# Kernel optimization log

Hardware: AMD Instinct MI355X
Metric: run time of the kernel (lower is better)

Reference implementation:

```python
import jax, jax.numpy as jnp
import numpy as np

N_ATOMS = 100000; E_ATOMS = 200000; N_AMINO = 10240; E_AMINO = 20480; B = 512
D_IN = 40; D_E = 11; H1 = 20; H2 = 20; H3 = 20; D_AA = 8; H_ARMA = 128; K = 3; T = 7
F1 = 256; F2 = 128; F3 = 64


def setup_inputs() -> dict:
    key = jax.random.key(0)
    ks = jax.random.split(key, 40)
    s = 0.05
    inp = {}
    inp['x'] = jax.random.normal(ks[0], (N_ATOMS, D_IN), dtype=jnp.float32)
    inp['edge_index'] = jax.random.randint(ks[1], (2, E_ATOMS), 0, N_ATOMS, dtype=jnp.int32)
    inp['edge_attr'] = jax.random.normal(ks[2], (E_ATOMS, D_E), dtype=jnp.float32)
    inp['monomer_labels'] = jax.random.randint(ks[3], (N_ATOMS,), 0, N_AMINO, dtype=jnp.int32)
    inp['aminoacids_features'] = jax.random.normal(ks[4], (N_AMINO, D_AA), dtype=jnp.float32)
    inp['amino_edge_index'] = jax.random.randint(ks[5], (2, E_AMINO), 0, N_AMINO, dtype=jnp.int32)
    inp['amino_batch'] = jnp.sort(jax.random.randint(ks[6], (N_AMINO,), 0, B, dtype=jnp.int32))
    # NNConv params: edge-MLP (Linear(D_E, in*out)), root weight, bias
    inp['nn1_w'] = jax.random.normal(ks[7], (D_E, D_IN * H1)) * s
    inp['nn1_b'] = jax.random.normal(ks[8], (D_IN * H1,)) * s
    inp['root1'] = jax.random.normal(ks[9], (D_IN, H1)) * s
    inp['b1'] = jax.random.normal(ks[10], (H1,)) * s
    inp['nn2_w'] = jax.random.normal(ks[11], (D_E, H1 * H2)) * s
    inp['nn2_b'] = jax.random.normal(ks[12], (H1 * H2,)) * s
    inp['root2'] = jax.random.normal(ks[13], (H1, H2)) * s
    inp['b2'] = jax.random.normal(ks[14], (H2,)) * s
    inp['nn3_w'] = jax.random.normal(ks[15], (D_E, H2 * H3)) * s
    inp['nn3_b'] = jax.random.normal(ks[16], (H2 * H3,)) * s
    inp['root3'] = jax.random.normal(ks[17], (H2, H3)) * s
    inp['b3'] = jax.random.normal(ks[18], (H3,)) * s
    # ARMAConv params (K stacks, T layers, shared_weights=False)
    F_ARMA_IN = H3 + D_AA
    inp['arma_init'] = jax.random.normal(ks[19], (K, F_ARMA_IN, H_ARMA)) * s
    inp['arma_w'] = jax.random.normal(ks[20], (T - 1, K, H_ARMA, H_ARMA)) * s
    inp['arma_root'] = jax.random.normal(ks[21], (T, K, F_ARMA_IN, H_ARMA)) * s
    inp['arma_bias'] = jax.random.normal(ks[22], (T, K, 1, H_ARMA)) * s
    # FCN head
    inp['l1_w'] = jax.random.normal(ks[23], (H_ARMA, F1)) * s
    inp['l1_b'] = jax.random.normal(ks[24], (F1,)) * s
    inp['l2_w'] = jax.random.normal(ks[25], (F1, F2)) * s
    inp['l2_b'] = jax.random.normal(ks[26], (F2,)) * s
    inp['l3_w'] = jax.random.normal(ks[27], (F2, F3)) * s
    inp['l3_b'] = jax.random.normal(ks[28], (F3,)) * s
    inp['l4_w'] = jax.random.normal(ks[29], (F3, 1)) * s
    inp['l4_b'] = jax.random.normal(ks[30], (1,)) * s
    return inp


def _nnconv(x, ei, ea, w_nn, b_nn, root, bias, out_dim):
    # PyG NNConv (aggr='add'): out_i = x_i @ root + sum_{j->i} x_j @ W(e_ji) + bias
    E, d_in = ea.shape[0], x.shape[1]
    W = (ea @ w_nn + b_nn).reshape(E, d_in, out_dim)  # per-edge weight matrices
    msg = jnp.einsum('ei,eio->eo', x[ei[0]], W)       # gather + batched matvec
    agg = jax.ops.segment_sum(msg, ei[1], num_segments=x.shape[0])
    return x @ root + agg + bias


def _arma(x, ei, init_w, w, root_w, bias):
    # PyG ARMAConv: sym-normalized adjacency (no self loops), K stacks, T layers, ReLU act
    N = x.shape[0]
    deg = jax.ops.segment_sum(jnp.ones(ei.shape[1], x.dtype), ei[1], num_segments=N)
    dinv = jnp.where(deg > 0, deg ** -0.5, 0.0)
    norm = dinv[ei[0]] * dinv[ei[1]]  # [E_amino]
    out = None
    for t in range(T):
        h = jnp.einsum('nf,kfo->kno', x, init_w) if t == 0 else jnp.einsum('knf,kfo->kno', out, w[t - 1])
        msg = h[:, ei[0], :] * norm[None, :, None]
        h = jax.vmap(lambda m: jax.ops.segment_sum(m, ei[1], num_segments=N))(msg)
        h = h + jnp.einsum('nf,kfo->kno', x, root_w[t]) + bias[t]
        out = jax.nn.relu(h)
    return out.mean(0)  # mean over stacks


def reference(x, edge_index, edge_attr, monomer_labels, aminoacids_features,
              amino_edge_index, amino_batch,
              nn1_w, nn1_b, root1, b1, nn2_w, nn2_b, root2, b2, nn3_w, nn3_b, root3, b3,
              arma_init, arma_w, arma_root, arma_bias,
              l1_w, l1_b, l2_w, l2_b, l3_w, l3_b, l4_w, l4_b):
    h = jax.nn.relu(_nnconv(x, edge_index, edge_attr, nn1_w, nn1_b, root1, b1, H1))
    h = jax.nn.relu(_nnconv(h, edge_index, edge_attr, nn2_w, nn2_b, root2, b2, H2))
    h = jax.nn.relu(_nnconv(h, edge_index, edge_attr, nn3_w, nn3_b, root3, b3, H3))
    # per-graph loop flattened: atoms -> amino-acid sum readout (graphs disjoint)
    aa = jax.ops.segment_sum(h, monomer_labels, num_segments=N_AMINO)
    aa = jnp.concatenate([aa, aminoacids_features], axis=1)  # [N_AMINO, H3+8]
    aa = jax.nn.relu(_arma(aa, amino_edge_index, arma_init, arma_w, arma_root, arma_bias))
    g = jax.ops.segment_sum(aa, amino_batch, num_segments=B)  # per-graph sum readout
    p = jax.nn.relu(g @ l1_w + l1_b)  # dropout is identity in eval mode
    p = jax.nn.relu(p @ l2_w + l2_b)
    p = jax.nn.relu(p @ l3_w + l3_b)
    return (p @ l4_w + l4_b).reshape(-1)
```

## Files before the change

### kernel.cpp

```cpp
#include <hip/hip_runtime.h>

#define N_ATOMS 100000
#define E_ATOMS 200000
#define N_AMINO 10240
#define E_AMINO 20480
#define NGRAPH 512
#define DIN0 40
#define D_E 11
#define HD 20
#define D_AA 8
#define HA 128
#define KS 3
#define TL 7
#define F1 256
#define F2 128
#define F3 64
#define NTILE 16
#define ECAP 64
#define EAW 12

typedef unsigned short u16;
typedef unsigned int u32;
typedef __attribute__((ext_vector_type(8))) short short8;
typedef __attribute__((ext_vector_type(4))) float f32x4;

__device__ __forceinline__ float b2f(u16 u) {
    union { u32 i; float f; } v; v.i = ((u32)u) << 16; return v.f;
}
__device__ __forceinline__ u16 f2b(float f) {
    union { float f; u32 i; } v; v.f = f;
    u32 x = v.i;
    return (u16)((x + (((x >> 16) & 1u) + 0x7fffu)) >> 16);
}

#define MB1_ELEMS 15360
#define MB2_ELEMS 7680
#define PREP0_N (MB1_ELEMS + 2 * MB2_ELEMS + N_AMINO * D_AA + 2 * N_ATOMS + 2 * N_AMINO)
__global__ __launch_bounds__(256) void k_prep0(
    const float* __restrict__ w1, const float* __restrict__ b1,
    const float* __restrict__ w2, const float* __restrict__ b2,
    const float* __restrict__ w3, const float* __restrict__ b3,
    u16* __restrict__ Mb1, u16* __restrict__ Mb2, u16* __restrict__ Mb3,
    const float* __restrict__ af, float* __restrict__ aa,
    int* __restrict__ cs, int* __restrict__ cd,
    int* __restrict__ ca, int* __restrict__ cl) {
    int t = blockIdx.x * 256 + threadIdx.x;
    if (t < MB1_ELEMS) {
        int kb = t / 7680, rem = t % 7680;
        int c = rem >> 5, qj = rem & 31;
        int krow = kb * 32 + qj;
        float v = 0.f;
        if (krow < DIN0)
            v = (c < 220) ? w1[(c / 20) * 800 + krow * 20 + (c % 20)]
                          : b1[krow * 20 + (c - 220)];
        Mb1[t] = f2b(v);
    } else if (t < MB1_ELEMS + MB2_ELEMS) {
        int tt = t - MB1_ELEMS;
        int c = tt >> 5, qj = tt & 31;
        float v = 0.f;
        if (qj < HD)
            v = (c < 220) ? w2[(c / 20) * 400 + qj * 20 + (c % 20)]
                          : b2[qj * 20 + (c - 220)];
        Mb2[tt] = f2b(v);
    } else if (t < MB1_ELEMS + 2 * MB2_ELEMS) {
        int tt = t - MB1_ELEMS - MB2_ELEMS;
        int c = tt >> 5, qj = tt & 31;
        float v = 0.f;
        if (qj < HD)
            v = (c < 220) ? w3[(c / 20) * 400 + qj * 20 + (c % 20)]
                          : b3[qj * 20 + (c - 220)];
        Mb3[tt] = f2b(v);
    } else if (t < MB1_ELEMS + 2 * MB2_ELEMS + N_AMINO * D_AA) {
        int idx = t - MB1_ELEMS - 2 * MB2_ELEMS, m = idx / D_AA, j = idx % D_AA;
        aa[m * 28 + HD + j] = af[idx];
    } else {
        int z = t - MB1_ELEMS - 2 * MB2_ELEMS - N_AMINO * D_AA;
        if (z < N_ATOMS) cs[z] = 0;
        else if (z < 2 * N_ATOMS) cd[z - N_ATOMS] = 0;
        else if (z < 2 * N_ATOMS + N_AMINO) ca[z - 2 * N_ATOMS] = 0;
        else if (z < 2 * N_ATOMS + 2 * N_AMINO) cl[z - 2 * N_ATOMS - N_AMINO] = 0;
    }
}

#define WP0_ELEMS (KS * 8192)
#define WP1_ELEMS (6 * KS * 20480)
__global__ __launch_bounds__(256) void k_cvtwp2(
    const float* __restrict__ ai, const float* __restrict__ aw,
    const float* __restrict__ arw, u16* __restrict__ Wp) {
    int g = blockIdx.x * 256 + threadIdx.x;
    if (g < WP0_ELEMS) {
        int k = g / 8192, r = g % 8192;
        int kb = r >> 12, rem = r & 4095;
        int c = rem >> 5, qj = rem & 31;
        int krow = kb * 32 + qj;
        float v = 0.f;
        if (krow < 28)      v = ai[((size_t)k * 28 + krow) * HA + c];
        else if (krow < 56) v = arw[((size_t)k * 28 + (krow - 28)) * HA + c];
        Wp[g] = f2b(v);
    } else if (g < WP0_ELEMS + WP1_ELEMS) {
        int gg = g - WP0_ELEMS;
        int mat = gg / 20480, r = gg % 20480;
        int kb = r / 4096, rem = r & 4095;
        int c = rem >> 5, qj = rem & 31;
        int krow = kb * 32 + qj;
        int tm1 = mat / KS, k = mat % KS;
        float v = 0.f;
        if (krow < 128)      v = aw[((size_t)mat * 128 + krow) * HA + c];
        else if (krow < 156) v = arw[(((size_t)(tm1 + 1) * KS + k) * 28 + (krow - 128)) * HA + c];
        Wp[g] = f2b(v);
    }
}

#define NBS 98
#define NBA 10

__global__ __launch_bounds__(256) void k_csr_count(
    const int* __restrict__ esrc, const int* __restrict__ edst,
    const int* __restrict__ adst, const int* __restrict__ lbl,
    int* __restrict__ cs, int* __restrict__ cd,
    int* __restrict__ ca, int* __restrict__ cl) {
    int t = blockIdx.x * 256 + threadIdx.x;
    if (t < E_ATOMS) atomicAdd(cs + esrc[t], 1);
    else if (t < 2 * E_ATOMS) atomicAdd(cd + edst[t - E_ATOMS], 1);
    else if (t < 2 * E_ATOMS + E_AMINO) atomicAdd(ca + adst[t - 2 * E_ATOMS], 1);
    else if (t < 2 * E_ATOMS + E_AMINO + N_ATOMS) atomicAdd(cl + lbl[t - 2 * E_ATOMS - E_AMINO], 1);
}
__device__ __forceinline__ void seg_decode(int bx, int* blk, int* n, int* which) {
    if (bx < NBS)            { *which = 0; *blk = bx;             *n = N_ATOMS; }
    else if (bx < 2 * NBS)   { *which = 1; *blk = bx - NBS;       *n = N_ATOMS; }
    else if (bx < 2 * NBS + NBA) { *which = 2; *blk = bx - 2 * NBS; *n = N_AMINO; }
    else                     { *which = 3; *blk = bx - 2 * NBS - NBA; *n = N_AMINO; }
}
__global__ __launch_bounds__(256) void k_scan1(
    const int* __restrict__ cs, int* __restrict__ soff,
    const int* __restrict__ cd, int* __restrict__ doff,
    const int* __restrict__ ca, int* __restrict__ aoff,
    const int* __restrict__ cl, int* __restrict__ loff,
    int* __restrict__ bsum) {
    int blk, n, which;
    seg_decode(blockIdx.x, &blk, &n, &which);
    const int* c = which == 0 ? cs : which == 1 ? cd : which == 2 ? ca : cl;
    int* o = which == 0 ? soff : which == 1 ? doff : which == 2 ? aoff : loff;
    int tx = threadIdx.x, lane = tx & 63, w = tx >> 6;
    int i0 = blk * 1024 + tx * 4;
    int v[4];
#pragma unroll
    for (int q = 0; q < 4; ++q) v[q] = (i0 + q < n) ? c[i0 + q] : 0;
    int s = v[0] + v[1] + v[2] + v[3];
    int inc = s;
#pragma unroll
    for (int d = 1; d < 64; d <<= 1) {
        int u = __shfl_up(inc, d, 64);
        if (lane >= d) inc += u;
    }
    __shared__ int wsum[4];
    if (lane == 63) wsum[w] = inc;
    __syncthreads();
    int wo = 0;
    for (int i = 0; i < w; ++i) wo += wsum[i];
    int run = wo + inc - s;
#pragma unroll
    for (int q = 0; q < 4; ++q) {
        if (i0 + q < n) o[i0 + q] = run;
        run += v[q];
    }
    if (tx == 255) bsum[blockIdx.x] = wo + inc;
}
__global__ __launch_bounds__(128) void k_scan2(
    int* __restrict__ bsum, int* __restrict__ soff, int* __restrict__ doff,
    int* __restrict__ aoff, int* __restrict__ loff) {
    int bx = blockIdx.x;
    int nb   = (bx < 2) ? NBS : NBA;
    int base = (bx == 0) ? 0 : (bx == 1) ? NBS : (bx == 2) ? 2 * NBS : 2 * NBS + NBA;
    int* b = bsum + base;
    int tx = threadIdx.x, lane = tx & 63;
    int v = (tx < nb) ? b[tx] : 0;
    int inc = v;
#pragma unroll
    for (int d = 1; d < 64; d <<= 1) {
        int u = __shfl_up(inc, d, 64);
        if (lane >= d) inc += u;
    }
    __shared__ int w0;
    if (tx == 63) w0 = inc;
    __syncthreads();
    int excl = inc - v + ((tx >= 64) ? w0 : 0);
    if (tx < nb) b[tx] = excl;
    if (tx == nb - 1) {
        int tot = excl + v;
        if (bx == 0) soff[N_ATOMS] = tot;
        else if (bx == 1) doff[N_ATOMS] = tot;
        else if (bx == 2) aoff[N_AMINO] = tot;
        else loff[N_AMINO] = tot;
    }
}
__global__ __launch_bounds__(256) void k_scan3(
    int* __restrict__ soff, int* __restrict__ doff,
    int* __restrict__ aoff, int* __restrict__ loff,
    const int* __restrict__ bsum,
    int* __restrict__ us, int* __restrict__ ud,
    int* __restrict__ ua, int* __restrict__ ul) {
    int blk, n, which;
    seg_decode(blockIdx.x, &blk, &n, &which);
    int* o = which == 0 ? soff : which == 1 ? doff : which == 2 ? aoff : loff;
    int* cu = which == 0 ? us : which == 1 ? ud : which == 2 ? ua : ul;
    int add = bsum[blockIdx.x];
    int i0 = blk * 1024 + threadIdx.x * 4;
#pragma unroll
    for (int q = 0; q < 4; ++q)
        if (i0 + q < n) { int val = o[i0 + q] + add; o[i0 + q] = val; cu[i0 + q] = val; }
}
__global__ __launch_bounds__(256) void k_csr_fill(
    const int* __restrict__ esrc, const int* __restrict__ edst,
    const float* __restrict__ ea,
    int* __restrict__ us, int* __restrict__ srcP, u16* __restrict__ eaP,
    int* __restrict__ ud, int* __restrict__ dslot,
    const int* __restrict__ aei, int* __restrict__ ua, int* __restrict__ aeid,
    const int* __restrict__ aoff, float* __restrict__ nrm,
    const int* __restrict__ lbl, int* __restrict__ ul, int* __restrict__ lnid) {
    int t = blockIdx.x * 256 + threadIdx.x;
    if (t < E_ATOMS) {
        int jj = atomicAdd(us + esrc[t], 1);
        srcP[jj] = esrc[t];
        const float* e0 = ea + (size_t)t * D_E;
        u16* e1 = eaP + (size_t)jj * EAW;
#pragma unroll
        for (int k = 0; k < D_E; ++k) e1[k] = f2b(e0[k]);
        e1[D_E] = f2b(1.0f);
        int p = atomicAdd(ud + edst[t], 1);
        dslot[p] = jj;
    } else if (t < E_ATOMS + E_AMINO) {
        int e = t - E_ATOMS;
        int p = atomicAdd(ua + aei[E_AMINO + e], 1);
        aeid[p] = e;
    } else if (t < E_ATOMS + 2 * E_AMINO) {
        int e = t - E_ATOMS - E_AMINO;
        int s = aei[e], d = aei[E_AMINO + e];
        int ds = aoff[s + 1] - aoff[s], dd = aoff[d + 1] - aoff[d];
        float a = ds > 0 ? rsqrtf((float)ds) : 0.f;
        float b = dd > 0 ? rsqrtf((float)dd) : 0.f;
        nrm[e] = a * b;
    } else if (t < E_ATOMS + 2 * E_AMINO + N_ATOMS) {
        int n = t - E_ATOMS - 2 * E_AMINO;
        int p = atomicAdd(ul + lbl[n], 1);
        lnid[p] = n;
    }
}

template <int DIN, int KB, bool RAW>
__global__ __launch_bounds__(256, 6) void nnconv_edge10(
    const void* __restrict__ xin, const u16* __restrict__ eaP,
    const int* __restrict__ srcP, const int* __restrict__ soff,
    const u16* __restrict__ Mb, u16* __restrict__ msg) {
    constexpr int KPAD = KB * 32;
    __shared__ __align__(16) float y3[NTILE * 240];
    __shared__ __align__(16) u16 As[NTILE * KPAD];
    __shared__ __align__(16) float eaS[ECAP * 12];
    __shared__ int srcS[ECAP];
    int tx = threadIdx.x;
    int n0 = blockIdx.x * NTILE;
    int j0 = soff[n0], j1 = soff[n0 + NTILE];
    for (int i = tx; i < NTILE * KPAD; i += 256) {
        int node = i / KPAD, k = i % KPAD;
        u16 v = 0;
        if (k < DIN)
            v = RAW ? f2b(((const float*)xin)[(size_t)(n0 + node) * DIN + k])
                    : ((const u16*)xin)[(size_t)(n0 + node) * DIN + k];
        As[i] = v;
    }
    {
        int cn0 = j1 - j0; if (cn0 > ECAP) cn0 = ECAP;
        for (int i = tx; i < cn0; i += 256) srcS[i] = srcP[j0 + i] - n0;
        const u32* eg = (const u32*)(eaP + (size_t)j0 * EAW);
        for (int i = tx; i < cn0 * 6; i += 256) {
            u32 pv = eg[i];
            eaS[2 * i]     = b2f((u16)(pv & 0xffff));
            eaS[2 * i + 1] = b2f((u16)(pv >> 16));
        }
    }
    __syncthreads();
    {
        int wave = tx >> 6, lane = tx & 63;
        int m = lane & 15, q = lane >> 4;
        short8 aF[KB];
#pragma unroll
        for (int kb = 0; kb < KB; ++kb)
            aF[kb] = *(const short8*)&As[m * KPAD + kb * 32 + q * 8];
        for (int ct = wave; ct < 15; ct += 4) {
            int c0 = ct * 16;
            f32x4 acc = {0.f, 0.f, 0.f, 0.f};
#pragma unroll
            for (int kb = 0; kb < KB; ++kb) {
                short8 bF = *(const short8*)(Mb + (size_t)kb * 7680 + (size_t)(c0 + m) * 32 + q * 8);
                acc = __builtin_amdgcn_mfma_f32_16x16x32_bf16(aF[kb], bF, acc, 0, 0, 0);
            }
            int c = c0 + m;
            int slot = (c < 220) ? (c % 20) * 12 + c / 20 : (c - 220) * 12 + 11;
#pragma unroll
            for (int r = 0; r < 4; ++r)
                y3[(q * 4 + r) * 240 + slot] = acc[r];
        }
    }
    __syncthreads();
    int c0 = j0;
    while (true) {
        int cn = j1 - c0; if (cn > ECAP) cn = ECAP;
        for (int p = tx; p < cn * 20; p += 256) {
            int e = p / 20, o = p - e * 20;
            const float4* ev = (const float4*)&eaS[e * 12];
            const float4* yr = (const float4*)&y3[srcS[e] * 240 + o * 12];
            float4 e0 = ev[0], e1 = ev[1], e2 = ev[2];
            float4 q0 = yr[0], q1 = yr[1], q2 = yr[2];
            float mv = e0.x * q0.x + e0.y * q0.y + e0.z * q0.z + e0.w * q0.w
                     + e1.x * q1.x + e1.y * q1.y + e1.z * q1.z + e1.w * q1.w
                     + e2.x * q2.x + e2.y * q2.y + e2.z * q2.z + e2.w * q2.w;
            msg[(size_t)(c0 + e) * 20 + o] = f2b(mv);
        }
        c0 += cn;
        if (c0 >= j1) break;
        __syncthreads();
        int cm = j1 - c0; if (cm > ECAP) cm = ECAP;
        for (int i = tx; i < cm; i += 256) srcS[i] = srcP[c0 + i] - n0;
        const u32* eg = (const u32*)(eaP + (size_t)c0 * EAW);
        for (int i = tx; i < cm * 6; i += 256) {
            u32 pv = eg[i];
            eaS[2 * i]     = b2f((u16)(pv & 0xffff));
            eaS[2 * i + 1] = b2f((u16)(pv >> 16));
        }
        __syncthreads();
    }
}

template <int DIN, bool RAW>
__global__ __launch_bounds__(256) void nnconv_reduce(
    const void* __restrict__ xin, const float* __restrict__ root,
    const float* __restrict__ bias, const int* __restrict__ doff,
    const int* __restrict__ dslot, const u16* __restrict__ msg,
    u16* __restrict__ hout) {
    __shared__ float Rl[DIN * HD + HD];
    for (int t = threadIdx.x; t < DIN * HD; t += 256) Rl[t] = root[t];
    if (threadIdx.x < HD) Rl[DIN * HD + threadIdx.x] = bias[threadIdx.x];
    __syncthreads();
    int t = blockIdx.x * 256 + threadIdx.x;
    if (t >= N_ATOMS * HD) return;
    int n = t / HD, o = t % HD;
    float acc = Rl[DIN * HD + o];
    int j1 = doff[n + 1];
    for (int j = doff[n]; j < j1; ++j)
        acc += b2f(msg[(size_t)dslot[j] * 20 + o]);
    const float* xf = (const float*)xin + (size_t)n * DIN;
    const u16*   xb = (const u16*)xin + (size_t)n * DIN;
#pragma unroll
    for (int i = 0; i < DIN; ++i)
        acc += (RAW ? xf[i] : b2f(xb[i])) * Rl[i * HD + o];
    hout[t] = f2b(fmaxf(acc, 0.f));
}

__global__ __launch_bounds__(256) void aa_gather(
    const u16* __restrict__ h3, const int* __restrict__ loff,
    const int* __restrict__ lnid, float* __restrict__ aa) {
    int t = blockIdx.x * 256 + threadIdx.x;
    if (t >= N_AMINO * HD) return;
    int m = t / HD, o = t % HD;
    float s = 0.f;
    int j1 = loff[m + 1];
    for (int j = loff[m]; j < j1; ++j)
        s += b2f(h3[(size_t)lnid[j] * HD + o]);
    aa[m * 28 + o] = s;
}

__global__ __launch_bounds__(256) void k_gaa(
    const float* __restrict__ aa, const int* __restrict__ aoff,
    const int* __restrict__ aeid, const int* __restrict__ aei,
    const float* __restrict__ nrm, u16* __restrict__ A0) {
    int t = blockIdx.x * 256 + threadIdx.x;
    if (t >= N_AMINO * 64) return;
    int n = t >> 6, c = t & 63;
    float v = 0.f;
    if (c < 28) {
        int j1 = aoff[n + 1];
        for (int jj = aoff[n]; jj < j1; ++jj) {
            int e = aeid[jj], s = aei[e];
            v += nrm[e] * aa[(size_t)s * 28 + c];
        }
    } else if (c < 56) {
        v = aa[(size_t)n * 28 + (c - 28)];
    }
    A0[t] = f2b(v);
}

__global__ __launch_bounds__(256) void arma_l0(
    const u16* __restrict__ A0, const u16* __restrict__ Wp0,
    const float* __restrict__ abi, u16* __restrict__ O, size_t kstride) {
    int wave = threadIdx.x >> 6, lane = threadIdx.x & 63;
    int k = blockIdx.y;
    const u16* W = Wp0 + (size_t)k * 8192;
    u16* Ok = O + (size_t)k * kstride;
    const float* bk = abi + (size_t)k * HA;
    int n0 = (blockIdx.x * 4 + wave) * 16;
    int m = lane & 15, q = lane >> 4;
    short8 aF[2];
#pragma unroll
    for (int kb = 0; kb < 2; ++kb)
        aF[kb] = *(const short8*)(A0 + (size_t)(n0 + m) * 64 + kb * 32 + q * 8);
#pragma unroll
    for (int ct = 0; ct < 8; ++ct) {
        int c0 = ct * 16;
        float b = bk[c0 + m];
        f32x4 acc = {b, b, b, b};
#pragma unroll
        for (int kb = 0; kb < 2; ++kb) {
            short8 bF = *(const short8*)(W + (size_t)((kb * 128 + c0 + m) * 32 + q * 8));
            acc = __builtin_amdgcn_mfma_f32_16x16x32_bf16(aF[kb], bF, acc, 0, 0, 0);
        }
#pragma unroll
        for (int r = 0; r < 4; ++r)
            Ok[(size_t)(n0 + q * 4 + r) * HA + c0 + m] = f2b(fmaxf(acc[r], 0.f));
    }
}

__global__ __launch_bounds__(256) void arma_lt(
    const u16* __restrict__ Oprev, const u16* __restrict__ Wm,
    const float* __restrict__ abit, const float* __restrict__ aa,
    const int* __restrict__ aoff, const int* __restrict__ aeid,
    const int* __restrict__ aei, const float* __restrict__ nrm,
    u16* __restrict__ Onext, size_t kstride) {
    __shared__ __align__(16) u16 As[64 * 160];
    int tx = threadIdx.x;
    int k = blockIdx.y;
    int n0b = blockIdx.x * 64;
    const u16* Op = Oprev + (size_t)k * kstride;
    const u16* W  = Wm + (size_t)k * 20480;
    for (int i = tx; i < 1024; i += 256) {
        int nl = i >> 4, cb = i & 15;
        int n = n0b + nl;
        int j1 = aoff[n + 1];
        float a0 = 0.f, a1 = 0.f, a2 = 0.f, a3 = 0.f;
        float a4 = 0.f, a5 = 0.f, a6 = 0.f, a7 = 0.f;
        for (int jj = aoff[n]; jj < j1; ++jj) {
            int e = aeid[jj], s = aei[e];
            float nm = nrm[e];
            uint4 hv = *(const uint4*)(Op + (size_t)s * HA + cb * 8);
            a0 += nm * b2f((u16)(hv.x & 0xffff));
            a1 += nm * b2f((u16)(hv.x >> 16));
            a2 += nm * b2f((u16)(hv.y & 0xffff));
            a3 += nm * b2f((u16)(hv.y >> 16));
            a4 += nm * b2f((u16)(hv.z & 0xffff));
            a5 += nm * b2f((u16)(hv.z >> 16));
            a6 += nm * b2f((u16)(hv.w & 0xffff));
            a7 += nm * b2f((u16)(hv.w >> 16));
        }
        uint4 pk;
        pk.x = (u32)f2b(a0) | ((u32)f2b(a1) << 16);
        pk.y = (u32)f2b(a2) | ((u32)f2b(a3) << 16);
        pk.z = (u32)f2b(a4) | ((u32)f2b(a5) << 16);
        pk.w = (u32)f2b(a6) | ((u32)f2b(a7) << 16);
        *(uint4*)&As[nl * 160 + cb * 8] = pk;
    }
    {
        int nl = tx >> 2, cb = tx & 3;
        int n = n0b + nl;
        float av[8];
#pragma unroll
        for (int j = 0; j < 8; ++j) {
            int c = cb * 8 + j;
            av[j] = (c < 28) ? aa[(size_t)n * 28 + c] : 0.f;
        }
        uint4 pk;
        pk.x = (u32)f2b(av[0]) | ((u32)f2b(av[1]) << 16);
        pk.y = (u32)f2b(av[2]) | ((u32)f2b(av[3]) << 16);
        pk.z = (u32)f2b(av[4]) | ((u32)f2b(av[5]) << 16);
        pk.w = (u32)f2b(av[6]) | ((u32)f2b(av[7]) << 16);
        *(uint4*)&As[nl * 160 + 128 + cb * 8] = pk;
    }
    __syncthreads();
    int wave = tx >> 6, lane = tx & 63;
    int m = lane & 15, q = lane >> 4;
    int wl = wave * 16 + m;
    short8 aF[5];
#pragma unroll
    for (int kb = 0; kb < 5; ++kb)
        aF[kb] = *(const short8*)&As[wl * 160 + kb * 32 + q * 8];
    int n0 = n0b + wave * 16;
    u16* On = Onext + (size_t)k * kstride;
    const float* bk = abit + (size_t)k * HA;
#pragma unroll
    for (int ct = 0; ct < 8; ++ct) {
        int c0 = ct * 16;
        float b = bk[c0 + m];
        f32x4 acc = {b, b, b, b};
#pragma unroll
        for (int kb = 0; kb < 5; ++kb) {
            short8 bF = *(const short8*)(W + (size_t)((kb * 128 + c0 + m) * 32 + q * 8));
            acc = __builtin_amdgcn_mfma_f32_16x16x32_bf16(aF[kb], bF, acc, 0, 0, 0);
        }
#pragma unroll
        for (int r = 0; r < 4; ++r)
            On[(size_t)(n0 + q * 4 + r) * HA + c0 + m] = f2b(fmaxf(acc[r], 0.f));
    }
}

__global__ __launch_bounds__(256) void head2(
    const u16* __restrict__ O, size_t kstride, const int* __restrict__ bat,
    const float* __restrict__ l1w, const float* __restrict__ l1b,
    const float* __restrict__ l2w, const float* __restrict__ l2b,
    const float* __restrict__ l3w, const float* __restrict__ l3b,
    const float* __restrict__ l4w, const float* __restrict__ l4b,
    float* __restrict__ outp) {
    __shared__ float sg[HA], sp1[F1], sp2[F2], sp3[F3];
    int b = blockIdx.x, tx = threadIdx.x;
    int lo = 0, hi = N_AMINO;
    while (lo < hi) { int mid = (lo + hi) >> 1; if (bat[mid] < b) lo = mid + 1; else hi = mid; }
    int s = lo;
    lo = 0; hi = N_AMINO;
    while (lo < hi) { int mid = (lo + hi) >> 1; if (bat[mid] < b + 1) lo = mid + 1; else hi = mid; }
    int e = lo;
    if (tx < HA) {
        float acc = 0.f;
        for (int n = s; n < e; ++n)
            acc += b2f(O[(size_t)n * HA + tx]) + b2f(O[kstride + (size_t)n * HA + tx])
                 + b2f(O[2 * kstride + (size_t)n * HA + tx]);
        sg[tx] = acc * (1.f / 3.f);
    }
    __syncthreads();
    {   float acc = l1b[tx];
        for (int f = 0; f < HA; ++f) acc += sg[f] * l1w[f * F1 + tx];
        sp1[tx] = fmaxf(acc, 0.f); }
    __syncthreads();
    if (tx < F2) {
        float acc = l2b[tx];
        for (int f = 0; f < F1; ++f) acc += sp1[f] * l2w[f * F2 + tx];
        sp2[tx] = fmaxf(acc, 0.f); }
    __syncthreads();
    if (tx < F3) {
        float acc = l3b[tx];
        for (int f = 0; f < F2; ++f) acc += sp2[f] * l3w[f * F3 + tx];
        sp3[tx] = fmaxf(acc, 0.f); }
    __syncthreads();
    if (tx < 64) {
        float p = sp3[tx] * l4w[tx];
        for (int off = 32; off > 0; off >>= 1) p += __shfl_down(p, off, 64);
        if (tx == 0) outp[b] = p + l4b[0];
    }
}

#define OFF_M1    ((size_t)0)
#define OFF_M2    ((size_t)38400)
#define OFF_M3    ((size_t)57600)
#define OFF_AOFF  ((size_t)76800)
#define OFF_AEID  ((size_t)118016)
#define OFF_NRM   ((size_t)199936)
#define OFF_AA    ((size_t)281856)
#define OFF_HA    ((size_t)2891008)
#define OFF_HB    ((size_t)6891008)
#define OFF_MSG   ((size_t)10891008)
#define OFF_SOFF  ((size_t)18891008)
#define OFF_DOFF  ((size_t)19291136)
#define OFF_DSLOT ((size_t)19691264)
#define OFF_LOFF  ((size_t)20491264)
#define OFF_LNID  ((size_t)20532480)
#define OFF_CS    ((size_t)20932480)
#define OFF_CD    ((size_t)21332480)
#define OFF_CA    ((size_t)21732480)
#define OFF_CL    ((size_t)21773440)
#define OFF_US    ((size_t)21814400)
#define OFF_UD    ((size_t)22214400)
#define OFF_UA    ((size_t)22614400)
#define OFF_UL    ((size_t)22655360)
#define OFF_BSUM  ((size_t)22696320)
#define OFF_EAP   ((size_t)22697216)
#define OFF_SRCP  ((size_t)27497216)
#define OFF_WP    ((size_t)28297216)
#define OFF_OB    ((size_t)2891008)
#define OFF_A0    ((size_t)10891008)
#define OFF_OA    ((size_t)18619648)

extern "C" void kernel_launch(void* const* d_in, const int* in_sizes, int n_in,
                              void* d_out, int out_size, void* d_ws, size_t ws_size,
                              hipStream_t stream) {
    (void)in_sizes; (void)n_in; (void)out_size; (void)ws_size;
    const float* x   = (const float*)d_in[0];
    const int*   ei  = (const int*)d_in[1];
    const float* ea  = (const float*)d_in[2];
    const int*   lbl = (const int*)d_in[3];
    const float* af  = (const float*)d_in[4];
    const int*   aei = (const int*)d_in[5];
    const int*   bat = (const int*)d_in[6];
    const float* nn1w = (const float*)d_in[7];  const float* nn1b = (const float*)d_in[8];
    const float* rt1  = (const float*)d_in[9];  const float* b1   = (const float*)d_in[10];
    const float* nn2w = (const float*)d_in[11]; const float* nn2b = (const float*)d_in[12];
    const float* rt2  = (const float*)d_in[13]; const float* b2   = (const float*)d_in[14];
    const float* nn3w = (const float*)d_in[15]; const float* nn3b = (const float*)d_in[16];
    const float* rt3  = (const float*)d_in[17]; const float* b3   = (const float*)d_in[18];
    const float* ai   = (const float*)d_in[19]; const float* aw   = (const float*)d_in[20];
    const float* arw  = (const float*)d_in[21]; const float* abi  = (const float*)d_in[22];
    const float* l1w  = (const float*)d_in[23]; const float* l1b  = (const float*)d_in[24];
    const float* l2w  = (const float*)d_in[25]; const float* l2b  = (const float*)d_in[26];
    const float* l3w  = (const float*)d_in[27]; const float* l3b  = (const float*)d_in[28];
    const float* l4w  = (const float*)d_in[29]; const float* l4b  = (const float*)d_in[30];
    float* outp = (float*)d_out;

    char* ws = (char*)d_ws;
    u16*   Mb1   = (u16*)(ws + OFF_M1);
    u16*   Mb2   = (u16*)(ws + OFF_M2);
    u16*   Mb3   = (u16*)(ws + OFF_M3);
    int*   aoff  = (int*)(ws + OFF_AOFF);
    int*   aeid  = (int*)(ws + OFF_AEID);
    float* nrm   = (float*)(ws + OFF_NRM);
    float* aa    = (float*)(ws + OFF_AA);
    u16*   hA    = (u16*)(ws + OFF_HA);
    u16*   hB    = (u16*)(ws + OFF_HB);
    u16*   msg   = (u16*)(ws + OFF_MSG);
    int*   soff  = (int*)(ws + OFF_SOFF);
    int*   doff  = (int*)(ws + OFF_DOFF);
    int*   dslot = (int*)(ws + OFF_DSLOT);
    int*   loff  = (int*)(ws + OFF_LOFF);
    int*   lnid  = (int*)(ws + OFF_LNID);
    int*   cs    = (int*)(ws + OFF_CS);
    int*   cd    = (int*)(ws + OFF_CD);
    int*   ca    = (int*)(ws + OFF_CA);
    int*   cl    = (int*)(ws + OFF_CL);
    int*   us    = (int*)(ws + OFF_US);
    int*   ud    = (int*)(ws + OFF_UD);
    int*   ua    = (int*)(ws + OFF_UA);
    int*   ul    = (int*)(ws + OFF_UL);
    int*   bsum  = (int*)(ws + OFF_BSUM);
    u16*   eaP   = (u16*)(ws + OFF_EAP);
    int*   srcP  = (int*)(ws + OFF_SRCP);
    u16*   Wp    = (u16*)(ws + OFF_WP);
    u16*   A0    = (u16*)(ws + OFF_A0);
    u16*   OA    = (u16*)(ws + OFF_OA);
    u16*   OB    = (u16*)(ws + OFF_OB);

    const int* esrc = ei;
    const int* edst = ei + E_ATOMS;
    const int* adst = aei + E_AMINO;

    k_prep0<<<(PREP0_N + 255) / 256, 256, 0, stream>>>(
        nn1w, nn1b, nn2w, nn2b, nn3w, nn3b, Mb1, Mb2, Mb3, af, aa, cs, cd, ca, cl);
    k_cvtwp2<<<(WP0_ELEMS + WP1_ELEMS + 255) / 256, 256, 0, stream>>>(ai, aw, arw, Wp);
    k_csr_count<<<(2 * E_ATOMS + E_AMINO + N_ATOMS + 255) / 256, 256, 0, stream>>>(
        esrc, edst, adst, lbl, cs, cd, ca, cl);
    k_scan1<<<2 * NBS + 2 * NBA, 256, 0, stream>>>(cs, soff, cd, doff, ca, aoff, cl, loff, bsum);
    k_scan2<<<4, 128, 0, stream>>>(bsum, soff, doff, aoff, loff);
    k_scan3<<<2 * NBS + 2 * NBA, 256, 0, stream>>>(soff, doff, aoff, loff, bsum, us, ud, ua, ul);
    k_csr_fill<<<(E_ATOMS + 2 * E_AMINO + N_ATOMS + 255) / 256, 256, 0, stream>>>(
        esrc, edst, ea, us, srcP, eaP, ud, dslot, aei, ua, aeid, aoff, nrm, lbl, ul, lnid);

    const int GT = N_ATOMS / NTILE;
    const int GF = (N_ATOMS * HD + 255) / 256;
    nnconv_edge10<DIN0, 2, true ><<<GT, 256, 0, stream>>>(x,  eaP, srcP, soff, Mb1, msg);
    nnconv_reduce<DIN0, true ><<<GF, 256, 0, stream>>>(x,  rt1, b1, doff, dslot, msg, hA);
    nnconv_edge10<HD,   1, false><<<GT, 256, 0, stream>>>(hA, eaP, srcP, soff, Mb2, msg);
    nnconv_reduce<HD,   false><<<GF, 256, 0, stream>>>(hA, rt2, b2, doff, dslot, msg, hB);
    nnconv_edge10<HD,   1, false><<<GT, 256, 0, stream>>>(hB, eaP, srcP, soff, Mb3, msg);
    nnconv_reduce<HD,   false><<<GF, 256, 0, stream>>>(hB, rt3, b3, doff, dslot, msg, hA);
    aa_gather<<<(N_AMINO * HD + 255) / 256, 256, 0, stream>>>(hA, loff, lnid, aa);

    const size_t KH = (size_t)N_AMINO * HA;
    k_gaa<<<(N_AMINO * 64 + 255) / 256, 256, 0, stream>>>(aa, aoff, aeid, aei, nrm, A0);
    arma_l0<<<dim3(160, KS), 256, 0, stream>>>(A0, Wp, abi, OA, KH);
    for (int t = 1; t < TL; ++t) {
        const u16* Oin  = (t & 1) ? OA : OB;
        u16*       Oout = (t & 1) ? OB : OA;
        arma_lt<<<dim3(160, KS), 256, 0, stream>>>(
            Oin, Wp + WP0_ELEMS + (size_t)((t - 1) * KS) * 20480,
            abi + (size_t)t * KS * HA, aa, aoff, aeid, aei, nrm, Oout, KH);
    }
    head2<<<NGRAPH, 256, 0, stream>>>(OA, KH, bat, l1w, l1b, l2w, l2b,
                                      l3w, l3b, l4w, l4b, outp);
}
```

Before: 506.4 us.

## Fold root-weight transform into edge MFMA and write messages in destination order

Adds the root weight as an extra 20-column block in the per-layer MFMA weight matrix, so the edge kernel computes the self term plus bias per node and writes it to a new buffer. The reduce kernel no longer reloads node features or does the root dot product. Edge messages are now scattered straight to their destination-sorted slot (the CSR fill records each edge's slot), so the reduce reads messages contiguously instead of through an indirection array. The costs are two extra MFMA column tiles per edge block, scattered writes in the edge kernel, and the self term being rounded to bf16 before accumulation.

After: 469.3 us. 1.08x faster.

```diff
diff --git a/kernel.cpp b/kernel.cpp
--- a/kernel.cpp
+++ b/kernel.cpp
@@ -33,42 +33,48 @@
     return (u16)((x + (((x >> 16) & 1u) + 0x7fffu)) >> 16);
 }
 
-#define MB1_ELEMS 15360
-#define MB2_ELEMS 7680
+#define MB1_ELEMS 17408
+#define MB2_ELEMS 8704
 #define PREP0_N (MB1_ELEMS + 2 * MB2_ELEMS + N_AMINO * D_AA + 2 * N_ATOMS + 2 * N_AMINO)
 __global__ __launch_bounds__(256) void k_prep0(
-    const float* __restrict__ w1, const float* __restrict__ b1,
-    const float* __restrict__ w2, const float* __restrict__ b2,
-    const float* __restrict__ w3, const float* __restrict__ b3,
+    const float* __restrict__ w1, const float* __restrict__ nb1, const float* __restrict__ r1,
+    const float* __restrict__ w2, const float* __restrict__ nb2, const float* __restrict__ r2,
+    const float* __restrict__ w3, const float* __restrict__ nb3, const float* __restrict__ r3,
     u16* __restrict__ Mb1, u16* __restrict__ Mb2, u16* __restrict__ Mb3,
     const float* __restrict__ af, float* __restrict__ aa,
     int* __restrict__ cs, int* __restrict__ cd,
     int* __restrict__ ca, int* __restrict__ cl) {
     int t = blockIdx.x * 256 + threadIdx.x;
     if (t < MB1_ELEMS) {
-        int kb = t / 7680, rem = t % 7680;
+        int kb = t / 8704, rem = t % 8704;
         int c = rem >> 5, qj = rem & 31;
         int krow = kb * 32 + qj;
         float v = 0.f;
-        if (krow < DIN0)
-            v = (c < 220) ? w1[(c / 20) * 800 + krow * 20 + (c % 20)]
-                          : b1[krow * 20 + (c - 220)];
+        if (krow < DIN0) {
+            if (c < 220)      v = w1[(c / 20) * 800 + krow * 20 + (c % 20)];
+            else if (c < 240) v = nb1[krow * 20 + (c - 220)];
+            else if (c < 260) v = r1[krow * 20 + (c - 240)];
+        }
         Mb1[t] = f2b(v);
     } else if (t < MB1_ELEMS + MB2_ELEMS) {
         int tt = t - MB1_ELEMS;
         int c = tt >> 5, qj = tt & 31;
         float v = 0.f;
-        if (qj < HD)
-            v = (c < 220) ? w2[(c / 20) * 400 + qj * 20 + (c % 20)]
-                          : b2[qj * 20 + (c - 220)];
+        if (qj < HD) {
+            if (c < 220)      v = w2[(c / 20) * 400 + qj * 20 + (c % 20)];
+            else if (c < 240) v = nb2[qj * 20 + (c - 220)];
+            else if (c < 260) v = r2[qj * 20 + (c - 240)];
+        }
         Mb2[tt] = f2b(v);
     } else if (t < MB1_ELEMS + 2 * MB2_ELEMS) {
         int tt = t - MB1_ELEMS - MB2_ELEMS;
         int c = tt >> 5, qj = tt & 31;
         float v = 0.f;
-        if (qj < HD)
-            v = (c < 220) ? w3[(c / 20) * 400 + qj * 20 + (c % 20)]
-                          : b3[qj * 20 + (c - 220)];
+        if (qj < HD) {
+            if (c < 220)      v = w3[(c / 20) * 400 + qj * 20 + (c % 20)];
+            else if (c < 240) v = nb3[qj * 20 + (c - 220)];
+            else if (c < 260) v = r3[qj * 20 + (c - 240)];
+        }
         Mb3[tt] = f2b(v);
     } else if (t < MB1_ELEMS + 2 * MB2_ELEMS + N_AMINO * D_AA) {
         int idx = t - MB1_ELEMS - 2 * MB2_ELEMS, m = idx / D_AA, j = idx % D_AA;
@@ -214,7 +220,7 @@
     const int* __restrict__ esrc, const int* __restrict__ edst,
     const float* __restrict__ ea,
     int* __restrict__ us, int* __restrict__ srcP, u16* __restrict__ eaP,
-    int* __restrict__ ud, int* __restrict__ dslot,
+    int* __restrict__ ud, int* __restrict__ sdp,
     const int* __restrict__ aei, int* __restrict__ ua, int* __restrict__ aeid,
     const int* __restrict__ aoff, float* __restrict__ nrm,
     const int* __restrict__ lbl, int* __restrict__ ul, int* __restrict__ lnid) {
@@ -227,8 +233,7 @@
 #pragma unroll
         for (int k = 0; k < D_E; ++k) e1[k] = f2b(e0[k]);
         e1[D_E] = f2b(1.0f);
-        int p = atomicAdd(ud + edst[t], 1);
-        dslot[p] = jj;
+        sdp[jj] = atomicAdd(ud + edst[t], 1);
     } else if (t < E_ATOMS + E_AMINO) {
         int e = t - E_ATOMS;
         int p = atomicAdd(ua + aei[E_AMINO + e], 1);
@@ -248,15 +253,18 @@
 }
 
 template <int DIN, int KB, bool RAW>
-__global__ __launch_bounds__(256, 6) void nnconv_edge10(
+__global__ __launch_bounds__(256, 6) void nnconv_edge11(
     const void* __restrict__ xin, const u16* __restrict__ eaP,
-    const int* __restrict__ srcP, const int* __restrict__ soff,
-    const u16* __restrict__ Mb, u16* __restrict__ msg) {
+    const int* __restrict__ srcP, const int* __restrict__ sdp,
+    const int* __restrict__ soff, const u16* __restrict__ Mb,
+    const float* __restrict__ bnn, u16* __restrict__ msg,
+    u16* __restrict__ selfm) {
     constexpr int KPAD = KB * 32;
     __shared__ __align__(16) float y3[NTILE * 240];
     __shared__ __align__(16) u16 As[NTILE * KPAD];
     __shared__ __align__(16) float eaS[ECAP * 12];
     __shared__ int srcS[ECAP];
+    __shared__ int sdpS[ECAP];
     int tx = threadIdx.x;
     int n0 = blockIdx.x * NTILE;
     int j0 = soff[n0], j1 = soff[n0 + NTILE];
@@ -270,7 +278,10 @@
     }
     {
         int cn0 = j1 - j0; if (cn0 > ECAP) cn0 = ECAP;
-        for (int i = tx; i < cn0; i += 256) srcS[i] = srcP[j0 + i] - n0;
+        for (int i = tx; i < cn0; i += 256) {
+            srcS[i] = srcP[j0 + i] - n0;
+            sdpS[i] = sdp[j0 + i];
+        }
         const u32* eg = (const u32*)(eaP + (size_t)j0 * EAW);
         for (int i = tx; i < cn0 * 6; i += 256) {
             u32 pv = eg[i];
@@ -286,19 +297,26 @@
 #pragma unroll
         for (int kb = 0; kb < KB; ++kb)
             aF[kb] = *(const short8*)&As[m * KPAD + kb * 32 + q * 8];
-        for (int ct = wave; ct < 15; ct += 4) {
+        for (int ct = wave; ct < 17; ct += 4) {
             int c0 = ct * 16;
             f32x4 acc = {0.f, 0.f, 0.f, 0.f};
 #pragma unroll
             for (int kb = 0; kb < KB; ++kb) {
-                short8 bF = *(const short8*)(Mb + (size_t)kb * 7680 + (size_t)(c0 + m) * 32 + q * 8);
+                short8 bF = *(const short8*)(Mb + (size_t)kb * 8704 + (size_t)(c0 + m) * 32 + q * 8);
                 acc = __builtin_amdgcn_mfma_f32_16x16x32_bf16(aF[kb], bF, acc, 0, 0, 0);
             }
             int c = c0 + m;
-            int slot = (c < 220) ? (c % 20) * 12 + c / 20 : (c - 220) * 12 + 11;
-#pragma unroll
-            for (int r = 0; r < 4; ++r)
-                y3[(q * 4 + r) * 240 + slot] = acc[r];
+            if (c < 240) {
+                int slot = (c < 220) ? (c % 20) * 12 + c / 20 : (c - 220) * 12 + 11;
+#pragma unroll
+                for (int r = 0; r < 4; ++r)
+                    y3[(q * 4 + r) * 240 + slot] = acc[r];
+            } else if (c < 260) {
+                float bv = bnn[c - 240];
+#pragma unroll
+                for (int r = 0; r < 4; ++r)
+                    selfm[(size_t)(n0 + q * 4 + r) * 20 + (c - 240)] = f2b(acc[r] + bv);
+            }
         }
     }
     __syncthreads();
@@ -314,13 +332,16 @@
             float mv = e0.x * q0.x + e0.y * q0.y + e0.z * q0.z + e0.w * q0.w
                      + e1.x * q1.x + e1.y * q1.y + e1.z * q1.z + e1.w * q1.w
                      + e2.x * q2.x + e2.y * q2.y + e2.z * q2.z + e2.w * q2.w;
-            msg[(size_t)(c0 + e) * 20 + o] = f2b(mv);
+            msg[(size_t)sdpS[e] * 20 + o] = f2b(mv);
         }
         c0 += cn;
         if (c0 >= j1) break;
         __syncthreads();
         int cm = j1 - c0; if (cm > ECAP) cm = ECAP;
-        for (int i = tx; i < cm; i += 256) srcS[i] = srcP[c0 + i] - n0;
+        for (int i = tx; i < cm; i += 256) {
+            srcS[i] = srcP[c0 + i] - n0;
+            sdpS[i] = sdp[c0 + i];
+        }
         const u32* eg = (const u32*)(eaP + (size_t)c0 * EAW);
         for (int i = tx; i < cm * 6; i += 256) {
             u32 pv = eg[i];
@@ -331,28 +352,16 @@
     }
 }
 
-template <int DIN, bool RAW>
-__global__ __launch_bounds__(256) void nnconv_reduce(
-    const void* __restrict__ xin, const float* __restrict__ root,
-    const float* __restrict__ bias, const int* __restrict__ doff,
-    const int* __restrict__ dslot, const u16* __restrict__ msg,
-    u16* __restrict__ hout) {
-    __shared__ float Rl[DIN * HD + HD];
-    for (int t = threadIdx.x; t < DIN * HD; t += 256) Rl[t] = root[t];
-    if (threadIdx.x < HD) Rl[DIN * HD + threadIdx.x] = bias[threadIdx.x];
-    __syncthreads();
+__global__ __launch_bounds__(256) void nnconv_reduce2(
+    const u16* __restrict__ selfm, const int* __restrict__ doff,
+    const u16* __restrict__ msg, u16* __restrict__ hout) {
     int t = blockIdx.x * 256 + threadIdx.x;
     if (t >= N_ATOMS * HD) return;
-    int n = t / HD, o = t % HD;
-    float acc = Rl[DIN * HD + o];
+    int n = t / HD, o = t - n * HD;
+    float acc = b2f(selfm[t]);
     int j1 = doff[n + 1];
     for (int j = doff[n]; j < j1; ++j)
-        acc += b2f(msg[(size_t)dslot[j] * 20 + o]);
-    const float* xf = (const float*)xin + (size_t)n * DIN;
-    const u16*   xb = (const u16*)xin + (size_t)n * DIN;
-#pragma unroll
-    for (int i = 0; i < DIN; ++i)
-        acc += (RAW ? xf[i] : b2f(xb[i])) * Rl[i * HD + o];
+        acc += b2f(msg[(size_t)j * HD + o]);
     hout[t] = f2b(fmaxf(acc, 0.f));
 }
 
@@ -571,6 +580,7 @@
 #define OFF_EAP   ((size_t)22697216)
 #define OFF_SRCP  ((size_t)27497216)
 #define OFF_WP    ((size_t)28297216)
+#define OFF_SELFM ((size_t)29083648)
 #define OFF_OB    ((size_t)2891008)
 #define OFF_A0    ((size_t)10891008)
 #define OFF_OA    ((size_t)18619648)
@@ -613,7 +623,7 @@
     u16*   msg   = (u16*)(ws + OFF_MSG);
     int*   soff  = (int*)(ws + OFF_SOFF);
     int*   doff  = (int*)(ws + OFF_DOFF);
-    int*   dslot = (int*)(ws + OFF_DSLOT);
+    int*   sdp   = (int*)(ws + OFF_DSLOT);
     int*   loff  = (int*)(ws + OFF_LOFF);
     int*   lnid  = (int*)(ws + OFF_LNID);
     int*   cs    = (int*)(ws + OFF_CS);
@@ -628,6 +638,7 @@
     u16*   eaP   = (u16*)(ws + OFF_EAP);
     int*   srcP  = (int*)(ws + OFF_SRCP);
     u16*   Wp    = (u16*)(ws + OFF_WP);
+    u16*   selfm = (u16*)(ws + OFF_SELFM);
     u16*   A0    = (u16*)(ws + OFF_A0);
     u16*   OA    = (u16*)(ws + OFF_OA);
     u16*   OB    = (u16*)(ws + OFF_OB);
@@ -637,7 +648,8 @@
     const int* adst = aei + E_AMINO;
 
     k_prep0<<<(PREP0_N + 255) / 256, 256, 0, stream>>>(
-        nn1w, nn1b, nn2w, nn2b, nn3w, nn3b, Mb1, Mb2, Mb3, af, aa, cs, cd, ca, cl);
+        nn1w, nn1b, rt1, nn2w, nn2b, rt2, nn3w, nn3b, rt3,
+        Mb1, Mb2, Mb3, af, aa, cs, cd, ca, cl);
     k_cvtwp2<<<(WP0_ELEMS + WP1_ELEMS + 255) / 256, 256, 0, stream>>>(ai, aw, arw, Wp);
     k_csr_count<<<(2 * E_ATOMS + E_AMINO + N_ATOMS + 255) / 256, 256, 0, stream>>>(
         esrc, edst, adst, lbl, cs, cd, ca, cl);
@@ -645,16 +657,16 @@
     k_scan2<<<4, 128, 0, stream>>>(bsum, soff, doff, aoff, loff);
     k_scan3<<<2 * NBS + 2 * NBA, 256, 0, stream>>>(soff, doff, aoff, loff, bsum, us, ud, ua, ul);
     k_csr_fill<<<(E_ATOMS + 2 * E_AMINO + N_ATOMS + 255) / 256, 256, 0, stream>>>(
-        esrc, edst, ea, us, srcP, eaP, ud, dslot, aei, ua, aeid, aoff, nrm, lbl, ul, lnid);
+        esrc, edst, ea, us, srcP, eaP, ud, sdp, aei, ua, aeid, aoff, nrm, lbl, ul, lnid);
 
     const int GT = N_ATOMS / NTILE;
     const int GF = (N_ATOMS * HD + 255) / 256;
-    nnconv_edge10<DIN0, 2, true ><<<GT, 256, 0, stream>>>(x,  eaP, srcP, soff, Mb1, msg);
-    nnconv_reduce<DIN0, true ><<<GF, 256, 0, stream>>>(x,  rt1, b1, doff, dslot, msg, hA);
-    nnconv_edge10<HD,   1, false><<<GT, 256, 0, stream>>>(hA, eaP, srcP, soff, Mb2, msg);
-    nnconv_reduce<HD,   false><<<GF, 256, 0, stream>>>(hA, rt2, b2, doff, dslot, msg, hB);
-    nnconv_edge10<HD,   1, false><<<GT, 256, 0, stream>>>(hB, eaP, srcP, soff, Mb3, msg);
-    nnconv_reduce<HD,   false><<<GF, 256, 0, stream>>>(hB, rt3, b3, doff, dslot, msg, hA);
+    nnconv_edge11<DIN0, 2, true ><<<GT, 256, 0, stream>>>(x,  eaP, srcP, sdp, soff, Mb1, b1, msg, selfm);
+    nnconv_reduce2<<<GF, 256, 0, stream>>>(selfm, doff, msg, hA);
+    nnconv_edge11<HD,   1, false><<<GT, 256, 0, stream>>>(hA, eaP, srcP, sdp, soff, Mb2, b2, msg, selfm);
+    nnconv_reduce2<<<GF, 256, 0, stream>>>(selfm, doff, msg, hB);
+    nnconv_edge11<HD,   1, false><<<GT, 256, 0, stream>>>(hB, eaP, srcP, sdp, soff, Mb3, b3, msg, selfm);
+    nnconv_reduce2<<<GF, 256, 0, stream>>>(selfm, doff, msg, hA);
     aa_gather<<<(N_AMINO * HD + 255) / 256, 256, 0, stream>>>(hA, loff, lnid, aa);
 
     const size_t KH = (size_t)N_AMINO * HA;
```
